# Kernel tuning notes

Measured on AMD Instinct MI355X. Metric: run time of the kernel, lower is better.

The kernel has to match this reference:

```python
import jax, jax.numpy as jnp
import numpy as np

B, C, H, W = 32, 256, 64, 64
h, w = 8, 8          # partition size
S = 4                # num_sharesets
RED = 4              # globalperceptron_reduce
EPS = 1e-5           # BatchNorm eps


def setup_inputs() -> dict:
    key = jax.random.key(0)
    ks = jax.random.split(key, 20)
    Ci = C // RED
    def bn_params(i):
        return (1.0 + 0.1 * jax.random.normal(ks[i], (S,), jnp.float32),      # gamma
                0.1 * jax.random.normal(ks[i + 1], (S,), jnp.float32),        # beta
                0.1 * jax.random.normal(ks[i + 2], (S,), jnp.float32),        # running_mean
                jax.random.uniform(ks[i + 3], (S,), jnp.float32, 0.5, 1.5))   # running_var
    g3, b3, m3, v3 = bn_params(6)
    g1, b1, m1, v1 = bn_params(10)
    gk, bk, mk, vk = bn_params(14)
    return {
        "x": jax.random.normal(ks[0], (B, C, H, W), jnp.float32),
        # GlobalPerceptron (1x1 convs on pooled vector == dense layers)
        "fc1_w": 0.05 * jax.random.normal(ks[1], (Ci, C), jnp.float32),
        "fc1_b": jnp.zeros((Ci,), jnp.float32),
        "fc2_w": 0.05 * jax.random.normal(ks[2], (C, Ci), jnp.float32),
        "fc2_b": jnp.zeros((C,), jnp.float32),
        # fc3: grouped 1x1 conv over S*h*w channels -> S independent (h*w,h*w) mats
        "fc3_w": 0.05 * jax.random.normal(ks[3], (S, h * w, h * w), jnp.float32),
        "fc3bn_g": g3, "fc3bn_b": b3, "fc3bn_m": m3, "fc3bn_v": v3,
        # reparam depthwise conv branches (k=1 and k=3), groups=S
        "conv1_w": 0.1 * jax.random.normal(ks[4], (S, 1, 1, 1), jnp.float32),
        "bn1_g": g1, "bn1_b": b1, "bn1_m": m1, "bn1_v": v1,
        "conv3_w": 0.1 * jax.random.normal(ks[5], (S, 1, 3, 3), jnp.float32),
        "bn3_g": gk, "bn3_b": bk, "bn3_m": mk, "bn3_v": vk,
    }


def _bn(x, g, b, m, v):
    # inference-mode BatchNorm2d over channel dim 1 (S channels)
    scale = g / jnp.sqrt(v + EPS)
    return x * scale[None, :, None, None] + (b - m * scale)[None, :, None, None]


def _dwconv(x, wgt, k):
    # depthwise (groups=S) conv, stride 1, SAME-ish padding k//2
    return jax.lax.conv_general_dilated(
        x, wgt, (1, 1), [(k // 2, k // 2)] * 2,
        feature_group_count=S, dimension_numbers=("NCHW", "OIHW", "NCHW"))


def reference(x, fc1_w, fc1_b, fc2_w, fc2_b, fc3_w,
              fc3bn_g, fc3bn_b, fc3bn_m, fc3bn_v,
              conv1_w, bn1_g, bn1_b, bn1_m, bn1_v,
              conv3_w, bn3_g, bn3_b, bn3_m, bn3_v):
    hp, wp = H // h, W // w
    # GlobalPerceptron gate: avgpool -> fc -> relu -> fc -> sigmoid
    pooled = x.mean((2, 3))  # (B, C)
    gate = jax.nn.sigmoid(jnp.maximum(pooled @ fc1_w.T + fc1_b, 0.0) @ fc2_w.T + fc2_b)
    # partition: (B,C,H,W) -> (B,hp,wp,C,h,w)
    parts = x.reshape(B, C, hp, h, wp, w).transpose(0, 2, 4, 1, 3, 5)
    # fc3 grouped 1x1 conv: rows of S consecutive channels' (h*w) patches
    fc_in = parts.reshape(-1, S, h * w)                      # (B*hp*wp*C/S, S, h*w)
    fc3_out = jnp.einsum('nsi,soi->nso', fc_in, fc3_w).reshape(-1, S, h, w)
    fc3_out = _bn(fc3_out, fc3bn_g, fc3bn_b, fc3bn_m, fc3bn_v)
    # multi-branch depthwise convs on the same partitions, summed
    conv_in = parts.reshape(-1, S, h, w)
    conv_out = (_bn(_dwconv(conv_in, conv1_w, 1), bn1_g, bn1_b, bn1_m, bn1_v)
                + _bn(_dwconv(conv_in, conv3_w, 3), bn3_g, bn3_b, bn3_m, bn3_v))
    # merge, un-partition (literal translation of the torch reshape/permute chain)
    out = (fc3_out + conv_out).reshape(-1, hp, wp, S, h, w)
    out = out.transpose(0, 3, 1, 4, 2, 5).reshape(B, C, H, W)
    return out * gate[:, :, None, None]
```

## Files before the change

kernel.cpp:

```cpp
#include <hip/hip_runtime.h>
#include <hip/hip_bf16.h>
#include <math.h>

#define BN_EPS 1e-5f

typedef __attribute__((ext_vector_type(8))) short short8;
typedef __attribute__((ext_vector_type(4))) float f32x4;

__device__ __forceinline__ unsigned short bfbits(float f) {
  __hip_bfloat16 h = __float2bfloat16(f);
  return *reinterpret_cast<unsigned short*>(&h);
}
__device__ __forceinline__ float bf2f(unsigned short u) {
  union { unsigned v; float f; } c; c.v = ((unsigned)u) << 16;
  return c.f;
}

__global__ __launch_bounds__(256) void prep_pool_kernel(
    const float* __restrict__ x, float* __restrict__ pooled,
    const float* __restrict__ fc3_w,
    const float* __restrict__ g3, const float* __restrict__ b3,
    const float* __restrict__ m3, const float* __restrict__ v3,
    const float* __restrict__ c1w,
    const float* __restrict__ g1, const float* __restrict__ b1,
    const float* __restrict__ m1, const float* __restrict__ v1,
    const float* __restrict__ c3w,
    const float* __restrict__ gk, const float* __restrict__ bk,
    const float* __restrict__ mk, const float* __restrict__ vk,
    unsigned short* __restrict__ ahi, unsigned short* __restrict__ alo,
    float* __restrict__ totb) {
  int bid = blockIdx.x;
  int tid = threadIdx.x;
  if (bid < 16) {
    int s = bid >> 2;
    int o = (bid & 3) * 16 + (tid >> 4);
    int kc = (tid & 15) * 4;
    float sc3 = g3[s] * rsqrtf(v3[s] + BN_EPS);
    float sc1 = g1[s] * rsqrtf(v1[s] + BN_EPS);
    float sck = gk[s] * rsqrtf(vk[s] + BN_EPS);
    float c0 = sc1 * c1w[s] + sck * c3w[s * 9 + 4];
    int oh = o >> 3, ow = o & 7;
    unsigned short H[4], L[4];
#pragma unroll
    for (int j = 0; j < 4; ++j) {
      int k = kc + j;
      int kh = k >> 3, kw = k & 7;
      float a = sc3 * fc3_w[(s * 64 + o) * 64 + k];
      int dy = kh - oh, dx = kw - ow;
      if (dy >= -1 && dy <= 1 && dx >= -1 && dx <= 1)
        a += (dy == 0 && dx == 0) ? c0 : sck * c3w[s * 9 + (dy + 1) * 3 + (dx + 1)];
      unsigned short h = bfbits(a);
      H[j] = h;
      L[j] = bfbits(a - bf2f(h));
    }
    size_t base = (size_t)(s * 64 + o) * 64 + kc;
    *(ushort4*)(ahi + base) = make_ushort4(H[0], H[1], H[2], H[3]);
    *(ushort4*)(alo + base) = make_ushort4(L[0], L[1], L[2], L[3]);
    if (bid == 0 && tid < 4) {
      int ss = tid;
      float s3 = g3[ss] * rsqrtf(v3[ss] + BN_EPS);
      float s1 = g1[ss] * rsqrtf(v1[ss] + BN_EPS);
      float sk = gk[ss] * rsqrtf(vk[ss] + BN_EPS);
      totb[ss] = (b3[ss] - m3[ss] * s3) + (b1[ss] - m1[ss] * s1) + (bk[ss] - mk[ss] * sk);
    }
    return;
  }
  int bc = bid - 16;
  const float4* xp = reinterpret_cast<const float4*>(x + (size_t)bc * 4096);
  float s = 0.f;
#pragma unroll
  for (int k = 0; k < 4; ++k) {
    float4 v = xp[k * 256 + tid];
    s += (v.x + v.y) + (v.z + v.w);
  }
#pragma unroll
  for (int m = 32; m >= 1; m >>= 1) s += __shfl_xor(s, m, 64);
  __shared__ float wsum[4];
  if ((tid & 63) == 0) wsum[tid >> 6] = s;
  __syncthreads();
  if (tid == 0) pooled[bc] = (wsum[0] + wsum[1] + wsum[2] + wsum[3]) * (1.f / 4096.f);
}

__global__ __launch_bounds__(256) void gate_kernel(const float* __restrict__ pooled,
                                                   const float* __restrict__ fc1_w,
                                                   const float* __restrict__ fc1_b,
                                                   const float* __restrict__ fc2_w,
                                                   const float* __restrict__ fc2_b,
                                                   float* __restrict__ gate) {
  int b = blockIdx.x;
  int tid = threadIdx.x;
  __shared__ float p[256];
  __shared__ float hbuf[64];
  p[tid] = pooled[b * 256 + tid];
  __syncthreads();
  if (tid < 64) {
    float a = fc1_b[tid];
    const float* wr = fc1_w + tid * 256;
#pragma unroll 8
    for (int c = 0; c < 256; ++c) a += p[c] * wr[c];
    hbuf[tid] = fmaxf(a, 0.f);
  }
  __syncthreads();
  float g = fc2_b[tid];
  const float* w2 = fc2_w + tid * 64;
#pragma unroll 8
  for (int j = 0; j < 64; ++j) g += hbuf[j] * w2[j];
  gate[b * 256 + tid] = 1.f / (1.f + expf(-g));
}

__global__ __launch_bounds__(256, 4) void main_kernel(
    const float* __restrict__ x,
    const unsigned short* __restrict__ ahi, const unsigned short* __restrict__ alo,
    const float* __restrict__ totb, const float* __restrict__ gate,
    float* __restrict__ out) {
  int bid = blockIdx.x;
  int sp  = bid & 1;
  int cgh = (bid >> 1) & 7;
  int hpi = (bid >> 4) & 7;
  int b   = bid >> 7;
  int tid = threadIdx.x;
  int s    = __builtin_amdgcn_readfirstlane(sp * 2 + ((tid >> 7) & 1));
  int half = __builtin_amdgcn_readfirstlane((tid >> 6) & 1);
  int r16 = tid & 15;
  int g   = (tid >> 4) & 3;

  float tb = totb[s];

  short8 Ah[2][2], Al[2][2];
#pragma unroll
  for (int oti = 0; oti < 2; ++oti)
#pragma unroll
    for (int kt = 0; kt < 2; ++kt) {
      size_t off = (size_t)(s * 64 + (half * 2 + oti) * 16 + r16) * 64 + kt * 32 + g * 8;
      Ah[kt][oti] = *(const short8*)(ahi + off);
      Al[kt][oti] = *(const short8*)(alo + off);
    }

  f32x4 acc[2][4];
#pragma unroll
  for (int i = 0; i < 2; ++i)
#pragma unroll
    for (int j = 0; j < 4; ++j) acc[i][j] = f32x4{0.f, 0.f, 0.f, 0.f};

#pragma unroll
  for (int kt = 0; kt < 2; ++kt) {
    f32x4 q0[4], q1[4];
#pragma unroll
    for (int nt = 0; nt < 4; ++nt) {
      int n2 = nt * 16 + r16;
      int c_in = (cgh * 8 + (n2 & 7)) * 4 + s;
      const float* bp = x + (size_t)(b * 256 + c_in) * 4096
                        + (hpi * 8 + kt * 4 + g) * 64 + (n2 >> 3) * 8;
      q0[nt] = *(const f32x4*)bp;
      q1[nt] = *(const f32x4*)(bp + 4);
    }
#pragma unroll
    for (int nt = 0; nt < 4; ++nt) {
      float fv[8] = {q0[nt].x, q0[nt].y, q0[nt].z, q0[nt].w,
                     q1[nt].x, q1[nt].y, q1[nt].z, q1[nt].w};
      union { unsigned short u[8]; short8 v; } BH, BL;
#pragma unroll
      for (int j = 0; j < 8; ++j) {
        unsigned short h = bfbits(fv[j]);
        BH.u[j] = h;
        BL.u[j] = bfbits(fv[j] - bf2f(h));
      }
#pragma unroll
      for (int oti = 0; oti < 2; ++oti) {
        acc[oti][nt] = __builtin_amdgcn_mfma_f32_16x16x32_bf16(Ah[kt][oti], BH.v, acc[oti][nt], 0, 0, 0);
        acc[oti][nt] = __builtin_amdgcn_mfma_f32_16x16x32_bf16(Ah[kt][oti], BL.v, acc[oti][nt], 0, 0, 0);
        acc[oti][nt] = __builtin_amdgcn_mfma_f32_16x16x32_bf16(Al[kt][oti], BH.v, acc[oti][nt], 0, 0, 0);
      }
    }
  }

#pragma unroll
  for (int nt = 0; nt < 4; ++nt) {
    int n2 = nt * 16 + r16;
    int c_out = hpi * 32 + (n2 >> 3) * 4 + s;
    float gmul = gate[b * 256 + c_out];
    float* outb = out + (size_t)(b * 256 + c_out) * 4096 + cgh * 8 * 64 + (n2 & 7) * 8;
#pragma unroll
    for (int oti = 0; oti < 2; ++oti) {
      f32x4 a = acc[oti][nt];
      int hh = (half * 2 + oti) * 2 + (g >> 1);
      int wo = (g & 1) * 4;
      f32x4 o4 = {(a.x + tb) * gmul, (a.y + tb) * gmul,
                  (a.z + tb) * gmul, (a.w + tb) * gmul};
      __builtin_nontemporal_store(o4, (f32x4*)(outb + hh * 64 + wo));
    }
  }
}

extern "C" void kernel_launch(void* const* d_in, const int* in_sizes, int n_in,
                              void* d_out, int out_size, void* d_ws, size_t ws_size,
                              hipStream_t stream) {
  const float* x     = (const float*)d_in[0];
  const float* fc1_w = (const float*)d_in[1];
  const float* fc1_b = (const float*)d_in[2];
  const float* fc2_w = (const float*)d_in[3];
  const float* fc2_b = (const float*)d_in[4];
  const float* fc3_w = (const float*)d_in[5];
  const float* g3  = (const float*)d_in[6];
  const float* b3  = (const float*)d_in[7];
  const float* m3  = (const float*)d_in[8];
  const float* v3  = (const float*)d_in[9];
  const float* c1w = (const float*)d_in[10];
  const float* g1  = (const float*)d_in[11];
  const float* b1  = (const float*)d_in[12];
  const float* m1  = (const float*)d_in[13];
  const float* v1  = (const float*)d_in[14];
  const float* c3w = (const float*)d_in[15];
  const float* gk  = (const float*)d_in[16];
  const float* bk  = (const float*)d_in[17];
  const float* mk  = (const float*)d_in[18];
  const float* vk  = (const float*)d_in[19];
  float* out = (float*)d_out;

  float* pooled = (float*)d_ws;
  float* gate   = pooled + 8192;
  unsigned short* ahi = (unsigned short*)(gate + 8192);
  unsigned short* alo = ahi + 16384;
  float* totb   = (float*)(alo + 16384);

  prep_pool_kernel<<<8208, 256, 0, stream>>>(x, pooled, fc3_w, g3, b3, m3, v3,
                                             c1w, g1, b1, m1, v1, c3w, gk, bk,
                                             mk, vk, ahi, alo, totb);
  gate_kernel<<<32, 256, 0, stream>>>(pooled, fc1_w, fc1_b, fc2_w, fc2_b, gate);
  main_kernel<<<4096, 256, 0, stream>>>(x, ahi, alo, totb, gate, out);
}
```

Before: 87.42 us.

## Fuse prep, pooling, gate and main GEMM into one cooperative persistent kernel

Replaces the three-kernel sequence (prep/pool, gate MLP, main MFMA kernel) with a single cooperative kernel of 1024 blocks. It pools, then does a grid-wide sync, then each block recomputes the gate MLP for its batch locally and handles four channel groups per block. The aim is to remove two launch boundaries and the tiny serial gate kernel. In exchange it pays for a grid sync, redundant gate computation in every block, and less parallelism per block. It falls back to the old path if occupancy is below 4 blocks per CU.

Result: no change. 86.89 us (-0.6%).

```diff
diff --git a/kernel.cpp b/kernel.cpp
--- a/kernel.cpp
+++ b/kernel.cpp
@@ -1,6 +1,9 @@
 #include <hip/hip_runtime.h>
+#include <hip/hip_cooperative_groups.h>
 #include <hip/hip_bf16.h>
 #include <math.h>
+
+namespace cg = cooperative_groups;
 
 #define BN_EPS 1e-5f
 
@@ -14,6 +17,188 @@
 __device__ __forceinline__ float bf2f(unsigned short u) {
   union { unsigned v; float f; } c; c.v = ((unsigned)u) << 16;
   return c.f;
+}
+
+__global__ __launch_bounds__(256, 4) void fused_kernel(
+    const float* __restrict__ x,
+    const float* __restrict__ fc1_w, const float* __restrict__ fc1_b,
+    const float* __restrict__ fc2_w, const float* __restrict__ fc2_b,
+    const float* __restrict__ fc3_w,
+    const float* __restrict__ g3, const float* __restrict__ b3,
+    const float* __restrict__ m3, const float* __restrict__ v3,
+    const float* __restrict__ c1w,
+    const float* __restrict__ g1, const float* __restrict__ b1,
+    const float* __restrict__ m1, const float* __restrict__ v1,
+    const float* __restrict__ c3w,
+    const float* __restrict__ gk, const float* __restrict__ bk,
+    const float* __restrict__ mk, const float* __restrict__ vk,
+    float* __restrict__ pooled, unsigned short* __restrict__ ahi,
+    unsigned short* __restrict__ alo, float* __restrict__ totb,
+    float* __restrict__ gate_unused, float* __restrict__ out) {
+  __shared__ float part[4][64];
+  __shared__ float hid[64];
+
+  int bid = blockIdx.x;
+  int tid = threadIdx.x;
+
+  if (bid < 16) {
+    int ps = bid >> 2;
+    int o = (bid & 3) * 16 + (tid >> 4);
+    int kc = (tid & 15) * 4;
+    float sc3 = g3[ps] * rsqrtf(v3[ps] + BN_EPS);
+    float sc1 = g1[ps] * rsqrtf(v1[ps] + BN_EPS);
+    float sck = gk[ps] * rsqrtf(vk[ps] + BN_EPS);
+    float c0 = sc1 * c1w[ps] + sck * c3w[ps * 9 + 4];
+    int oh = o >> 3, ow = o & 7;
+    unsigned short H[4], L[4];
+#pragma unroll
+    for (int j = 0; j < 4; ++j) {
+      int k = kc + j;
+      int kh = k >> 3, kw = k & 7;
+      float a = sc3 * fc3_w[(ps * 64 + o) * 64 + k];
+      int dy = kh - oh, dx = kw - ow;
+      if (dy >= -1 && dy <= 1 && dx >= -1 && dx <= 1)
+        a += (dy == 0 && dx == 0) ? c0 : sck * c3w[ps * 9 + (dy + 1) * 3 + (dx + 1)];
+      unsigned short h = bfbits(a);
+      H[j] = h;
+      L[j] = bfbits(a - bf2f(h));
+    }
+    size_t base = (size_t)(ps * 64 + o) * 64 + kc;
+    *(ushort4*)(ahi + base) = make_ushort4(H[0], H[1], H[2], H[3]);
+    *(ushort4*)(alo + base) = make_ushort4(L[0], L[1], L[2], L[3]);
+    if (bid == 0 && tid < 4) {
+      int ss = tid;
+      float s3 = g3[ss] * rsqrtf(v3[ss] + BN_EPS);
+      float s1 = g1[ss] * rsqrtf(v1[ss] + BN_EPS);
+      float sk = gk[ss] * rsqrtf(vk[ss] + BN_EPS);
+      totb[ss] = (b3[ss] - m3[ss] * s3) + (b1[ss] - m1[ss] * s1) + (bk[ss] - mk[ss] * sk);
+    }
+  }
+
+  {
+    int w = tid >> 6, lane = tid & 63;
+#pragma unroll
+    for (int p = 0; p < 2; ++p) {
+      int bc = bid * 8 + w * 2 + p;
+      const f32x4* xp = (const f32x4*)(x + (size_t)bc * 4096);
+      float ssum = 0.f;
+#pragma unroll
+      for (int i = 0; i < 16; ++i) {
+        f32x4 v = xp[i * 64 + lane];
+        ssum += (v.x + v.y) + (v.z + v.w);
+      }
+#pragma unroll
+      for (int m = 32; m >= 1; m >>= 1) ssum += __shfl_xor(ssum, m, 64);
+      if (lane == 0) pooled[bc] = ssum * (1.f / 4096.f);
+    }
+  }
+
+  cg::this_grid().sync();
+
+  int cq  = bid & 1;
+  int sp  = (bid >> 1) & 1;
+  int hpi = (bid >> 2) & 7;
+  int b   = bid >> 5;
+  int s    = __builtin_amdgcn_readfirstlane(sp * 2 + ((tid >> 7) & 1));
+  int half = __builtin_amdgcn_readfirstlane((tid >> 6) & 1);
+  int r16 = tid & 15;
+  int g   = (tid >> 4) & 3;
+
+  {
+    int hh = tid & 63, q = tid >> 6;
+    const float* pb = pooled + b * 256 + q * 64;
+    const float* wr = fc1_w + hh * 256 + q * 64;
+    float a = 0.f;
+#pragma unroll 16
+    for (int j = 0; j < 64; ++j) a += pb[j] * wr[j];
+    part[q][hh] = a;
+  }
+  __syncthreads();
+  if (tid < 64)
+    hid[tid] = fmaxf(part[0][tid] + part[1][tid] + part[2][tid] + part[3][tid] + fc1_b[tid], 0.f);
+  __syncthreads();
+
+  float gmul[4];
+#pragma unroll
+  for (int nt = 0; nt < 4; ++nt) {
+    int c_out = hpi * 32 + (nt * 2 + (r16 >> 3)) * 4 + s;
+    const float* w2 = fc2_w + c_out * 64;
+    float a = fc2_b[c_out];
+#pragma unroll 16
+    for (int j = 0; j < 64; ++j) a += hid[j] * w2[j];
+    gmul[nt] = 1.f / (1.f + expf(-a));
+  }
+
+  float tb = totb[s];
+
+  short8 Ah[2][2], Al[2][2];
+#pragma unroll
+  for (int oti = 0; oti < 2; ++oti)
+#pragma unroll
+    for (int kt = 0; kt < 2; ++kt) {
+      size_t off = (size_t)(s * 64 + (half * 2 + oti) * 16 + r16) * 64 + kt * 32 + g * 8;
+      Ah[kt][oti] = *(const short8*)(ahi + off);
+      Al[kt][oti] = *(const short8*)(alo + off);
+    }
+
+  for (int u = 0; u < 4; ++u) {
+    int cgh = cq * 4 + u;
+
+    f32x4 acc[2][4];
+#pragma unroll
+    for (int i = 0; i < 2; ++i)
+#pragma unroll
+      for (int j = 0; j < 4; ++j) acc[i][j] = f32x4{0.f, 0.f, 0.f, 0.f};
+
+#pragma unroll
+    for (int kt = 0; kt < 2; ++kt) {
+      f32x4 q0[4], q1[4];
+#pragma unroll
+      for (int nt = 0; nt < 4; ++nt) {
+        int n2 = nt * 16 + r16;
+        int c_in = (cgh * 8 + (n2 & 7)) * 4 + s;
+        const float* bp = x + (size_t)(b * 256 + c_in) * 4096
+                          + (hpi * 8 + kt * 4 + g) * 64 + (n2 >> 3) * 8;
+        q0[nt] = *(const f32x4*)bp;
+        q1[nt] = *(const f32x4*)(bp + 4);
+      }
+#pragma unroll
+      for (int nt = 0; nt < 4; ++nt) {
+        float fv[8] = {q0[nt].x, q0[nt].y, q0[nt].z, q0[nt].w,
+                       q1[nt].x, q1[nt].y, q1[nt].z, q1[nt].w};
+        union { unsigned short u16[8]; short8 v; } BH, BL;
+#pragma unroll
+        for (int j = 0; j < 8; ++j) {
+          unsigned short h = bfbits(fv[j]);
+          BH.u16[j] = h;
+          BL.u16[j] = bfbits(fv[j] - bf2f(h));
+        }
+#pragma unroll
+        for (int oti = 0; oti < 2; ++oti) {
+          acc[oti][nt] = __builtin_amdgcn_mfma_f32_16x16x32_bf16(Ah[kt][oti], BH.v, acc[oti][nt], 0, 0, 0);
+          acc[oti][nt] = __builtin_amdgcn_mfma_f32_16x16x32_bf16(Ah[kt][oti], BL.v, acc[oti][nt], 0, 0, 0);
+          acc[oti][nt] = __builtin_amdgcn_mfma_f32_16x16x32_bf16(Al[kt][oti], BH.v, acc[oti][nt], 0, 0, 0);
+        }
+      }
+    }
+
+#pragma unroll
+    for (int nt = 0; nt < 4; ++nt) {
+      int n2 = nt * 16 + r16;
+      int c_out = hpi * 32 + (n2 >> 3) * 4 + s;
+      float gm = gmul[nt];
+      float* outb = out + (size_t)(b * 256 + c_out) * 4096 + cgh * 8 * 64 + (n2 & 7) * 8;
+#pragma unroll
+      for (int oti = 0; oti < 2; ++oti) {
+        f32x4 a = acc[oti][nt];
+        int hh = (half * 2 + oti) * 2 + (g >> 1);
+        int wo = (g & 1) * 4;
+        f32x4 o4 = {(a.x + tb) * gm, (a.y + tb) * gm,
+                    (a.z + tb) * gm, (a.w + tb) * gm};
+        __builtin_nontemporal_store(o4, (f32x4*)(outb + hh * 64 + wo));
+      }
+    }
+  }
 }
 
 __global__ __launch_bounds__(256) void prep_pool_kernel(
@@ -123,9 +308,7 @@
   int half = __builtin_amdgcn_readfirstlane((tid >> 6) & 1);
   int r16 = tid & 15;
   int g   = (tid >> 4) & 3;
-
   float tb = totb[s];
-
   short8 Ah[2][2], Al[2][2];
 #pragma unroll
   for (int oti = 0; oti < 2; ++oti)
@@ -135,13 +318,11 @@
       Ah[kt][oti] = *(const short8*)(ahi + off);
       Al[kt][oti] = *(const short8*)(alo + off);
     }
-
   f32x4 acc[2][4];
 #pragma unroll
   for (int i = 0; i < 2; ++i)
 #pragma unroll
     for (int j = 0; j < 4; ++j) acc[i][j] = f32x4{0.f, 0.f, 0.f, 0.f};
-
 #pragma unroll
   for (int kt = 0; kt < 2; ++kt) {
     f32x4 q0[4], q1[4];
@@ -173,7 +354,6 @@
       }
     }
   }
-
 #pragma unroll
   for (int nt = 0; nt < 4; ++nt) {
     int n2 = nt * 16 + r16;
@@ -223,9 +403,24 @@
   unsigned short* alo = ahi + 16384;
   float* totb   = (float*)(alo + 16384);
 
-  prep_pool_kernel<<<8208, 256, 0, stream>>>(x, pooled, fc3_w, g3, b3, m3, v3,
-                                             c1w, g1, b1, m1, v1, c3w, gk, bk,
-                                             mk, vk, ahi, alo, totb);
-  gate_kernel<<<32, 256, 0, stream>>>(pooled, fc1_w, fc1_b, fc2_w, fc2_b, gate);
-  main_kernel<<<4096, 256, 0, stream>>>(x, ahi, alo, totb, gate, out);
-}
+  int maxB = 0;
+  hipOccupancyMaxActiveBlocksPerMultiprocessor(&maxB, fused_kernel, 256, 0);
+  if (maxB >= 4) {
+    void* args[] = {
+      (void*)&x, (void*)&fc1_w, (void*)&fc1_b, (void*)&fc2_w, (void*)&fc2_b,
+      (void*)&fc3_w, (void*)&g3, (void*)&b3, (void*)&m3, (void*)&v3,
+      (void*)&c1w, (void*)&g1, (void*)&b1, (void*)&m1, (void*)&v1,
+      (void*)&c3w, (void*)&gk, (void*)&bk, (void*)&mk, (void*)&vk,
+      (void*)&pooled, (void*)&ahi, (void*)&alo, (void*)&totb,
+      (void*)&gate, (void*)&out,
+    };
+    hipLaunchCooperativeKernel((void*)fused_kernel, dim3(1024), dim3(256),
+                               args, 0, stream);
+  } else {
+    prep_pool_kernel<<<8208, 256, 0, stream>>>(x, pooled, fc3_w, g3, b3, m3, v3,
+                                               c1w, g1, b1, m1, v1, c3w, gk, bk,
+                                               mk, vk, ahi, alo, totb);
+    gate_kernel<<<32, 256, 0, stream>>>(pooled, fc1_w, fc1_b, fc2_w, fc2_b, gate);
+    main_kernel<<<4096, 256, 0, stream>>>(x, ahi, alo, totb, gate, out);
+  }
+}
```

## Repartition main kernel work per wave and pool one channel per wave

Applied to the files above, without the earlier changes.

The pooling stage now gives each wave its own (b,c) channel, with 16 loads per lane and no shared-memory reduction or block barrier. That cuts the prep grid to a quarter of its former block count. The main kernel now gives each block a single shareset and splits output columns across waves, doubling the grid and halving per-wave MFMA tiles. All x loads and gate loads are hoisted ahead of the A-fragment loads so memory latency overlaps. The trade-off is more blocks, with the A matrices reloaded per block.

Result: slower. 98.87 us (+13.1%).

```diff
diff --git a/kernel.cpp b/kernel.cpp
--- a/kernel.cpp
+++ b/kernel.cpp
@@ -65,20 +65,18 @@
     }
     return;
   }
-  int bc = bid - 16;
-  const float4* xp = reinterpret_cast<const float4*>(x + (size_t)bc * 4096);
-  float s = 0.f;
-#pragma unroll
-  for (int k = 0; k < 4; ++k) {
-    float4 v = xp[k * 256 + tid];
-    s += (v.x + v.y) + (v.z + v.w);
-  }
-#pragma unroll
-  for (int m = 32; m >= 1; m >>= 1) s += __shfl_xor(s, m, 64);
-  __shared__ float wsum[4];
-  if ((tid & 63) == 0) wsum[tid >> 6] = s;
-  __syncthreads();
-  if (tid == 0) pooled[bc] = (wsum[0] + wsum[1] + wsum[2] + wsum[3]) * (1.f / 4096.f);
+  int w = tid >> 6, lane = tid & 63;
+  int bc = (bid - 16) * 4 + w;
+  const f32x4* xp = (const f32x4*)(x + (size_t)bc * 4096);
+  float ssum = 0.f;
+#pragma unroll
+  for (int i = 0; i < 16; ++i) {
+    f32x4 v = xp[i * 64 + lane];
+    ssum += (v.x + v.y) + (v.z + v.w);
+  }
+#pragma unroll
+  for (int m = 32; m >= 1; m >>= 1) ssum += __shfl_xor(ssum, m, 64);
+  if (lane == 0) pooled[bc] = ssum * (1.f / 4096.f);
 }
 
 __global__ __launch_bounds__(256) void gate_kernel(const float* __restrict__ pooled,
@@ -114,17 +112,29 @@
     const float* __restrict__ totb, const float* __restrict__ gate,
     float* __restrict__ out) {
   int bid = blockIdx.x;
-  int sp  = bid & 1;
-  int cgh = (bid >> 1) & 7;
-  int hpi = (bid >> 4) & 7;
-  int b   = bid >> 7;
+  int s   = bid & 3;
+  int cgh = (bid >> 2) & 7;
+  int hpi = (bid >> 5) & 7;
+  int b   = bid >> 8;
   int tid = threadIdx.x;
-  int s    = __builtin_amdgcn_readfirstlane(sp * 2 + ((tid >> 7) & 1));
-  int half = __builtin_amdgcn_readfirstlane((tid >> 6) & 1);
+  int wv  = tid >> 6;
+  int colhalf = __builtin_amdgcn_readfirstlane(wv & 1);
+  int half    = __builtin_amdgcn_readfirstlane(wv >> 1);
   int r16 = tid & 15;
   int g   = (tid >> 4) & 3;
 
-  float tb = totb[s];
+  f32x4 q[2][2][2];
+  int c_in = (cgh * 8 + (r16 & 7)) * 4 + s;
+  const float* xbase = x + (size_t)(b * 256 + c_in) * 4096;
+#pragma unroll
+  for (int kt = 0; kt < 2; ++kt)
+#pragma unroll
+    for (int nt = 0; nt < 2; ++nt) {
+      int wpi = (colhalf * 2 + nt) * 2 + (r16 >> 3);
+      const float* bp = xbase + (hpi * 8 + kt * 4 + g) * 64 + wpi * 8;
+      q[kt][nt][0] = *(const f32x4*)bp;
+      q[kt][nt][1] = *(const f32x4*)(bp + 4);
+    }
 
   short8 Ah[2][2], Al[2][2];
 #pragma unroll
@@ -136,34 +146,32 @@
       Al[kt][oti] = *(const short8*)(alo + off);
     }
 
-  f32x4 acc[2][4];
+  float gmul[2];
+#pragma unroll
+  for (int nt = 0; nt < 2; ++nt) {
+    int n2 = (colhalf * 2 + nt) * 16 + r16;
+    gmul[nt] = gate[b * 256 + hpi * 32 + (n2 >> 3) * 4 + s];
+  }
+  float tb = totb[s];
+
+  f32x4 acc[2][2];
 #pragma unroll
   for (int i = 0; i < 2; ++i)
 #pragma unroll
-    for (int j = 0; j < 4; ++j) acc[i][j] = f32x4{0.f, 0.f, 0.f, 0.f};
-
-#pragma unroll
-  for (int kt = 0; kt < 2; ++kt) {
-    f32x4 q0[4], q1[4];
-#pragma unroll
-    for (int nt = 0; nt < 4; ++nt) {
-      int n2 = nt * 16 + r16;
-      int c_in = (cgh * 8 + (n2 & 7)) * 4 + s;
-      const float* bp = x + (size_t)(b * 256 + c_in) * 4096
-                        + (hpi * 8 + kt * 4 + g) * 64 + (n2 >> 3) * 8;
-      q0[nt] = *(const f32x4*)bp;
-      q1[nt] = *(const f32x4*)(bp + 4);
-    }
-#pragma unroll
-    for (int nt = 0; nt < 4; ++nt) {
-      float fv[8] = {q0[nt].x, q0[nt].y, q0[nt].z, q0[nt].w,
-                     q1[nt].x, q1[nt].y, q1[nt].z, q1[nt].w};
-      union { unsigned short u[8]; short8 v; } BH, BL;
+    for (int j = 0; j < 2; ++j) acc[i][j] = f32x4{0.f, 0.f, 0.f, 0.f};
+
+#pragma unroll
+  for (int kt = 0; kt < 2; ++kt)
+#pragma unroll
+    for (int nt = 0; nt < 2; ++nt) {
+      float fv[8] = {q[kt][nt][0].x, q[kt][nt][0].y, q[kt][nt][0].z, q[kt][nt][0].w,
+                     q[kt][nt][1].x, q[kt][nt][1].y, q[kt][nt][1].z, q[kt][nt][1].w};
+      union { unsigned short u16[8]; short8 v; } BH, BL;
 #pragma unroll
       for (int j = 0; j < 8; ++j) {
         unsigned short h = bfbits(fv[j]);
-        BH.u[j] = h;
-        BL.u[j] = bfbits(fv[j] - bf2f(h));
+        BH.u16[j] = h;
+        BL.u16[j] = bfbits(fv[j] - bf2f(h));
       }
 #pragma unroll
       for (int oti = 0; oti < 2; ++oti) {
@@ -172,21 +180,20 @@
         acc[oti][nt] = __builtin_amdgcn_mfma_f32_16x16x32_bf16(Al[kt][oti], BH.v, acc[oti][nt], 0, 0, 0);
       }
     }
-  }
-
-#pragma unroll
-  for (int nt = 0; nt < 4; ++nt) {
-    int n2 = nt * 16 + r16;
+
+#pragma unroll
+  for (int nt = 0; nt < 2; ++nt) {
+    int n2 = (colhalf * 2 + nt) * 16 + r16;
     int c_out = hpi * 32 + (n2 >> 3) * 4 + s;
-    float gmul = gate[b * 256 + c_out];
+    float gm = gmul[nt];
     float* outb = out + (size_t)(b * 256 + c_out) * 4096 + cgh * 8 * 64 + (n2 & 7) * 8;
 #pragma unroll
     for (int oti = 0; oti < 2; ++oti) {
       f32x4 a = acc[oti][nt];
       int hh = (half * 2 + oti) * 2 + (g >> 1);
       int wo = (g & 1) * 4;
-      f32x4 o4 = {(a.x + tb) * gmul, (a.y + tb) * gmul,
-                  (a.z + tb) * gmul, (a.w + tb) * gmul};
+      f32x4 o4 = {(a.x + tb) * gm, (a.y + tb) * gm,
+                  (a.z + tb) * gm, (a.w + tb) * gm};
       __builtin_nontemporal_store(o4, (f32x4*)(outb + hh * 64 + wo));
     }
   }
@@ -223,9 +230,9 @@
   unsigned short* alo = ahi + 16384;
   float* totb   = (float*)(alo + 16384);
 
-  prep_pool_kernel<<<8208, 256, 0, stream>>>(x, pooled, fc3_w, g3, b3, m3, v3,
+  prep_pool_kernel<<<2064, 256, 0, stream>>>(x, pooled, fc3_w, g3, b3, m3, v3,
                                              c1w, g1, b1, m1, v1, c3w, gk, bk,
                                              mk, vk, ahi, alo, totb);
   gate_kernel<<<32, 256, 0, stream>>>(pooled, fc1_w, fc1_b, fc2_w, fc2_b, gate);
-  main_kernel<<<4096, 256, 0, stream>>>(x, ahi, alo, totb, gate, out);
-}
+  main_kernel<<<8192, 256, 0, stream>>>(x, ahi, alo, totb, gate, out);
+}
```
